# Kernel tuning notes

Measured on AMD Instinct MI355X. Metric: run time of the kernel, lower is better.

The kernel has to match this reference:

```python
import jax, jax.numpy as jnp
import numpy as np

NUM_HEADS = 8
NUM_LAYERS = 4
ATTN_DIM = 256
INPUT_DIM = 256
HEAD_DIM = ATTN_DIM // NUM_HEADS


def setup_inputs() -> dict:
    key = jax.random.key(0)
    ks = jax.random.split(key, 4)
    B, N = 32, 512
    agents_state = jax.random.normal(ks[0], (B, N, INPUT_DIM), dtype=jnp.float32)
    # normc_initializer(0.01): small std weights; bias zeros (torch default bias is
    # uniform but zeros suffice for a baseline; kept as explicit params)
    Wq = jax.random.normal(ks[1], (ATTN_DIM, INPUT_DIM), dtype=jnp.float32) * 0.01
    Wk = jax.random.normal(ks[2], (ATTN_DIM, INPUT_DIM), dtype=jnp.float32) * 0.01
    Wv = jax.random.normal(ks[3], (ATTN_DIM, INPUT_DIM), dtype=jnp.float32) * 0.01
    bq = jnp.zeros((ATTN_DIM,), dtype=jnp.float32)
    bk = jnp.zeros((ATTN_DIM,), dtype=jnp.float32)
    bv = jnp.zeros((ATTN_DIM,), dtype=jnp.float32)
    return {"agents_state": agents_state, "Wq": Wq, "bq": bq, "Wk": Wk, "bk": bk, "Wv": Wv, "bv": bv}


def _mha(q, k, v):
    # q: [B, N, D]; k, v: [B, M, D]
    B, N, _ = q.shape
    M = k.shape[1]
    qh = q.reshape(B, N, NUM_HEADS, HEAD_DIM)
    kh = k.reshape(B, M, NUM_HEADS, HEAD_DIM)
    vh = v.reshape(B, M, NUM_HEADS, HEAD_DIM)
    scores = jnp.einsum('bnhd,bmhd->bnhm', qh, kh) / np.float32(HEAD_DIM ** 0.5)
    attn = jax.nn.softmax(scores, axis=-1)
    out = jnp.einsum('bnhm,bmhd->bnhd', attn, vh)
    return out.reshape(B, N, ATTN_DIM)


def reference(agents_state, Wq, bq, Wk, bk, Wv, bv):
    queries = agents_state @ Wq.T + bq
    keys = agents_state @ Wk.T + bk
    values = agents_state @ Wv.T + bv
    attn_output = queries
    for _ in range(NUM_LAYERS):
        attn_output = attn_output + _mha(attn_output, keys, values)
    return attn_output
```

## Files before the change

kernel.cpp:

```cpp
#include <hip/hip_runtime.h>

typedef __bf16 bf16x8 __attribute__((ext_vector_type(8)));
typedef float  f32x4  __attribute__((ext_vector_type(4)));

#define K_SCALE 0.25505402682247326f

static __device__ __forceinline__ unsigned short f2bf(float f) {
  return __builtin_bit_cast(unsigned short, (__bf16)f);
}
static __device__ __forceinline__ f32x4 mfma16(bf16x8 a, bf16x8 b, f32x4 c) {
  return __builtin_amdgcn_mfma_f32_16x16x32_bf16(a, b, c, 0, 0, 0);
}

__global__ __launch_bounds__(256) void prep_kernel(
    const float* __restrict__ X,
    const float* __restrict__ Wq, const float* __restrict__ bq,
    const float* __restrict__ Wk, const float* __restrict__ bk,
    const float* __restrict__ Wv, const float* __restrict__ bv,
    unsigned short* __restrict__ Xb, unsigned short* __restrict__ Wf,
    float* __restrict__ bias) {
  int blk = blockIdx.x;
  if (blk < 1024) {
    int idx = blk * 4096 + threadIdx.x * 16;
    const float4* src = reinterpret_cast<const float4*>(X + idx);
    float4 f0 = src[0], f1 = src[1], f2 = src[2], f3 = src[3];
    bf16x8 h0, h1;
    h0[0]=(__bf16)f0.x; h0[1]=(__bf16)f0.y; h0[2]=(__bf16)f0.z; h0[3]=(__bf16)f0.w;
    h0[4]=(__bf16)f1.x; h0[5]=(__bf16)f1.y; h0[6]=(__bf16)f1.z; h0[7]=(__bf16)f1.w;
    h1[0]=(__bf16)f2.x; h1[1]=(__bf16)f2.y; h1[2]=(__bf16)f2.z; h1[3]=(__bf16)f2.w;
    h1[4]=(__bf16)f3.x; h1[5]=(__bf16)f3.y; h1[6]=(__bf16)f3.z; h1[7]=(__bf16)f3.w;
    *reinterpret_cast<bf16x8*>(Xb + idx) = h0;
    *reinterpret_cast<bf16x8*>(Xb + idx + 8) = h1;
    return;
  }
  if (blk == 1120) {
    int t = threadIdx.x;
#pragma unroll
    for (int kseg = 0; kseg < 3; ++kseg) {
      int i = kseg * 256 + t;
      float bb;
      if (i < 256)      bb = bq[i];
      else if (i < 512) bb = bk[i - 256] * K_SCALE;
      else              bb = bv[i - 512];
      bias[i] = bb;
    }
    return;
  }
  int fidx = (blk - 1024) * 256 + threadIdx.x;
  int lane = fidx & 63;
  int ks = (fidx >> 6) & 7;
  int ct = fidx >> 9;
  int n = ct * 16 + (lane & 15);
  int kk = ks * 32 + (lane >> 4) * 8;
  const float* src;
  float scale = 1.0f;
  if (n < 256)      src = Wq + n * 256 + kk;
  else if (n < 512) { src = Wk + (n - 256) * 256 + kk; scale = K_SCALE; }
  else              src = Wv + (n - 512) * 256 + kk;
  float4 f0 = reinterpret_cast<const float4*>(src)[0];
  float4 f1 = reinterpret_cast<const float4*>(src)[1];
  bf16x8 h;
  h[0] = (__bf16)(f0.x * scale); h[1] = (__bf16)(f0.y * scale);
  h[2] = (__bf16)(f0.z * scale); h[3] = (__bf16)(f0.w * scale);
  h[4] = (__bf16)(f1.x * scale); h[5] = (__bf16)(f1.y * scale);
  h[6] = (__bf16)(f1.z * scale); h[7] = (__bf16)(f1.w * scale);
  *reinterpret_cast<bf16x8*>(Wf + fidx * 8) = h;
}

__global__ __launch_bounds__(512, 4) void attn_kernel(
    const unsigned short* __restrict__ Xb, const unsigned short* __restrict__ Wf,
    const float* __restrict__ bias, float* __restrict__ Out) {
  __shared__ __align__(16) unsigned short Ks[16384];
  __shared__ __align__(16) unsigned short Vf[16384];
  const int tid = threadIdx.x;
  const int bh = blockIdx.x >> 1, seg = blockIdx.x & 1;
  const int b = bh >> 3, h = bh & 7;
  const int w = tid >> 6, lane = tid & 63, c = lane & 15, quad = lane >> 4;
  const f32x4 zf = {0.f, 0.f, 0.f, 0.f};
  const int kw = w * 64;
  f32x4 accK[2][4], accV[4][2];
#pragma unroll
  for (int dt = 0; dt < 2; ++dt)
#pragma unroll
    for (int kt = 0; kt < 4; ++kt) { accK[dt][kt] = zf; accV[kt][dt] = zf; }
#pragma unroll
  for (int ks = 0; ks < 8; ++ks) {
    bf16x8 bX[4];
#pragma unroll
    for (int kt = 0; kt < 4; ++kt)
      bX[kt] = *reinterpret_cast<const bf16x8*>(
          Xb + (b * 512 + kw + kt * 16 + c) * 256 + ks * 32 + quad * 8);
    bf16x8 aWk[2], aWv[2];
#pragma unroll
    for (int dt = 0; dt < 2; ++dt) {
      aWk[dt] = *reinterpret_cast<const bf16x8*>(
          Wf + (((16 + h * 2 + dt) * 8 + ks) * 64 + lane) * 8);
      aWv[dt] = *reinterpret_cast<const bf16x8*>(
          Wf + (((32 + h * 2 + dt) * 8 + ks) * 64 + lane) * 8);
    }
#pragma unroll
    for (int dt = 0; dt < 2; ++dt)
#pragma unroll
      for (int kt = 0; kt < 4; ++kt)
        accK[dt][kt] = mfma16(aWk[dt], bX[kt], accK[dt][kt]);
#pragma unroll
    for (int mt = 0; mt < 4; ++mt)
#pragma unroll
      for (int nt = 0; nt < 2; ++nt)
        accV[mt][nt] = mfma16(bX[mt], aWv[nt], accV[mt][nt]);
  }
#pragma unroll
  for (int dt = 0; dt < 2; ++dt) {
    f32x4 bk4 = *reinterpret_cast<const f32x4*>(bias + 256 + h * 32 + dt * 16 + quad * 4);
#pragma unroll
    for (int kt = 0; kt < 4; ++kt) {
      int n = kw + kt * 16 + c;
      int slot = quad ^ ((n >> 1) & 3);
      ushort4 pk;
      pk.x = f2bf(accK[dt][kt][0] + bk4[0]); pk.y = f2bf(accK[dt][kt][1] + bk4[1]);
      pk.z = f2bf(accK[dt][kt][2] + bk4[2]); pk.w = f2bf(accK[dt][kt][3] + bk4[3]);
      *reinterpret_cast<ushort4*>(&Ks[n * 32 + slot * 8 + dt * 4]) = pk;
    }
  }
#pragma unroll
  for (int nt = 0; nt < 2; ++nt) {
    float bv1 = bias[512 + h * 32 + nt * 16 + c];
#pragma unroll
    for (int mt = 0; mt < 4; ++mt) {
      ushort4 pk;
      pk.x = f2bf(accV[mt][nt][0] + bv1); pk.y = f2bf(accV[mt][nt][1] + bv1);
      pk.z = f2bf(accV[mt][nt][2] + bv1); pk.w = f2bf(accV[mt][nt][3] + bv1);
      *reinterpret_cast<ushort4*>(
          &Vf[((w * 2 + (mt >> 1)) * 2 + nt) * 512 + (quad * 16 + c) * 8 + (mt & 1) * 4]) = pk;
    }
  }
  const int rowq = seg * 256 + w * 32;
  f32x4 x[2][2] = {{zf, zf}, {zf, zf}};
#pragma unroll
  for (int ks = 0; ks < 8; ++ks) {
    bf16x8 bXq[2], aQ[2];
#pragma unroll
    for (int rg = 0; rg < 2; ++rg)
      bXq[rg] = *reinterpret_cast<const bf16x8*>(
          Xb + (b * 512 + rowq + rg * 16 + c) * 256 + ks * 32 + quad * 8);
#pragma unroll
    for (int tt = 0; tt < 2; ++tt)
      aQ[tt] = *reinterpret_cast<const bf16x8*>(
          Wf + (((h * 2 + tt) * 8 + ks) * 64 + lane) * 8);
#pragma unroll
    for (int rg = 0; rg < 2; ++rg)
#pragma unroll
      for (int tt = 0; tt < 2; ++tt)
        x[rg][tt] = mfma16(aQ[tt], bXq[rg], x[rg][tt]);
  }
#pragma unroll
  for (int tt = 0; tt < 2; ++tt) {
    f32x4 bq4 = *reinterpret_cast<const f32x4*>(bias + h * 32 + tt * 16 + quad * 4);
#pragma unroll
    for (int rg = 0; rg < 2; ++rg) x[rg][tt] += bq4;
  }
  __syncthreads();
  bf16x8 ones;
#pragma unroll
  for (int j = 0; j < 8; ++j) ones[j] = (__bf16)1.0f;
#pragma unroll 1
  for (int layer = 0; layer < 4; ++layer) {
    bf16x8 aq[2];
#pragma unroll
    for (int rg = 0; rg < 2; ++rg) {
      aq[rg][0] = (__bf16)x[rg][0][0]; aq[rg][1] = (__bf16)x[rg][0][1];
      aq[rg][2] = (__bf16)x[rg][0][2]; aq[rg][3] = (__bf16)x[rg][0][3];
      aq[rg][4] = (__bf16)x[rg][1][0]; aq[rg][5] = (__bf16)x[rg][1][1];
      aq[rg][6] = (__bf16)x[rg][1][2]; aq[rg][7] = (__bf16)x[rg][1][3];
    }
    f32x4 sacc[2] = {zf, zf};
    f32x4 O[2][2] = {{zf, zf}, {zf, zf}};
#pragma unroll 4
    for (int ch = 0; ch < 16; ++ch) {
      f32x4 S[2][2];
#pragma unroll
      for (int tt = 0; tt < 2; ++tt) {
        int n = (ch * 2 + tt) * 16 + c;
        bf16x8 kf = *reinterpret_cast<const bf16x8*>(
            &Ks[n * 32 + ((quad ^ ((n >> 1) & 3)) << 3)]);
#pragma unroll
        for (int rg = 0; rg < 2; ++rg) S[rg][tt] = mfma16(kf, aq[rg], zf);
      }
      bf16x8 ap[2];
#pragma unroll
      for (int rg = 0; rg < 2; ++rg) {
#pragma unroll
        for (int tt = 0; tt < 2; ++tt)
#pragma unroll
          for (int r = 0; r < 4; ++r)
            S[rg][tt][r] = __builtin_amdgcn_exp2f(S[rg][tt][r]);
        ap[rg][0] = (__bf16)S[rg][0][0]; ap[rg][1] = (__bf16)S[rg][0][1];
        ap[rg][2] = (__bf16)S[rg][0][2]; ap[rg][3] = (__bf16)S[rg][0][3];
        ap[rg][4] = (__bf16)S[rg][1][0]; ap[rg][5] = (__bf16)S[rg][1][1];
        ap[rg][6] = (__bf16)S[rg][1][2]; ap[rg][7] = (__bf16)S[rg][1][3];
        sacc[rg] = mfma16(ones, ap[rg], sacc[rg]);
      }
#pragma unroll
      for (int tt = 0; tt < 2; ++tt) {
        bf16x8 vf = *reinterpret_cast<const bf16x8*>(
            &Vf[((ch * 2 + tt) * 64 + lane) * 8]);
#pragma unroll
        for (int rg = 0; rg < 2; ++rg) O[rg][tt] = mfma16(vf, ap[rg], O[rg][tt]);
      }
    }
#pragma unroll
    for (int rg = 0; rg < 2; ++rg) {
      float inv = __builtin_amdgcn_rcpf(sacc[rg][0]);
#pragma unroll
      for (int tt = 0; tt < 2; ++tt)
#pragma unroll
        for (int r = 0; r < 4; ++r) x[rg][tt][r] += O[rg][tt][r] * inv;
    }
  }
#pragma unroll
  for (int rg = 0; rg < 2; ++rg)
#pragma unroll
    for (int tt = 0; tt < 2; ++tt)
      *reinterpret_cast<f32x4*>(
          Out + (b * 512 + rowq + rg * 16 + c) * 256 + h * 32 + tt * 16 + quad * 4) = x[rg][tt];
}

extern "C" void kernel_launch(void* const* d_in, const int* in_sizes, int n_in,
                              void* d_out, int out_size, void* d_ws, size_t ws_size,
                              hipStream_t stream) {
  const float* X  = (const float*)d_in[0];
  const float* Wq = (const float*)d_in[1];
  const float* bq = (const float*)d_in[2];
  const float* Wk = (const float*)d_in[3];
  const float* bk = (const float*)d_in[4];
  const float* Wv = (const float*)d_in[5];
  const float* bv = (const float*)d_in[6];
  char* ws = (char*)d_ws;
  unsigned short* Wf   = (unsigned short*)(ws);
  float*          bias = (float*)(ws + 393216);
  unsigned short* Xb   = (unsigned short*)(ws + 397312);
  float* out = (float*)d_out;
  prep_kernel<<<1121, 256, 0, stream>>>(X, Wq, bq, Wk, bk, Wv, bv, Xb, Wf, bias);
  attn_kernel<<<512, 512, 0, stream>>>(Xb, Wf, bias, out);
}
```

Baseline: 153.2 us.

## Split K/V projection into separate phases and remap block order by batch

The fused K and V projection loop becomes two sequential scoped phases separated by scheduling barriers, so each phase holds only one set of accumulators and register pressure drops under the 4-blocks-per-CU bound. This reloads the X tiles from global memory twice, once per phase. The block index mapping also changes so that consecutive blocks take different batches for the same head and segment, which alters L2 reuse of the weight tiles versus the X tiles.

```diff
diff --git a/kernel.cpp b/kernel.cpp
--- a/kernel.cpp
+++ b/kernel.cpp
@@ -73,67 +73,88 @@
   __shared__ __align__(16) unsigned short Ks[16384];
   __shared__ __align__(16) unsigned short Vf[16384];
   const int tid = threadIdx.x;
-  const int bh = blockIdx.x >> 1, seg = blockIdx.x & 1;
-  const int b = bh >> 3, h = bh & 7;
+  const int b = blockIdx.x & 31, hs = blockIdx.x >> 5;
+  const int h = hs >> 1, seg = hs & 1;
   const int w = tid >> 6, lane = tid & 63, c = lane & 15, quad = lane >> 4;
   const f32x4 zf = {0.f, 0.f, 0.f, 0.f};
   const int kw = w * 64;
-  f32x4 accK[2][4], accV[4][2];
-#pragma unroll
-  for (int dt = 0; dt < 2; ++dt)
-#pragma unroll
-    for (int kt = 0; kt < 4; ++kt) { accK[dt][kt] = zf; accV[kt][dt] = zf; }
-#pragma unroll
-  for (int ks = 0; ks < 8; ++ks) {
-    bf16x8 bX[4];
-#pragma unroll
-    for (int kt = 0; kt < 4; ++kt)
-      bX[kt] = *reinterpret_cast<const bf16x8*>(
-          Xb + (b * 512 + kw + kt * 16 + c) * 256 + ks * 32 + quad * 8);
-    bf16x8 aWk[2], aWv[2];
+  {
+    f32x4 accK[2][4];
+#pragma unroll
+    for (int dt = 0; dt < 2; ++dt)
+#pragma unroll
+      for (int kt = 0; kt < 4; ++kt) accK[dt][kt] = zf;
+#pragma unroll
+    for (int ks = 0; ks < 8; ++ks) {
+      bf16x8 bX[4];
+#pragma unroll
+      for (int kt = 0; kt < 4; ++kt)
+        bX[kt] = *reinterpret_cast<const bf16x8*>(
+            Xb + (b * 512 + kw + kt * 16 + c) * 256 + ks * 32 + quad * 8);
+      bf16x8 aWk[2];
+#pragma unroll
+      for (int dt = 0; dt < 2; ++dt)
+        aWk[dt] = *reinterpret_cast<const bf16x8*>(
+            Wf + (((16 + h * 2 + dt) * 8 + ks) * 64 + lane) * 8);
+#pragma unroll
+      for (int dt = 0; dt < 2; ++dt)
+#pragma unroll
+        for (int kt = 0; kt < 4; ++kt)
+          accK[dt][kt] = mfma16(aWk[dt], bX[kt], accK[dt][kt]);
+    }
 #pragma unroll
     for (int dt = 0; dt < 2; ++dt) {
-      aWk[dt] = *reinterpret_cast<const bf16x8*>(
-          Wf + (((16 + h * 2 + dt) * 8 + ks) * 64 + lane) * 8);
-      aWv[dt] = *reinterpret_cast<const bf16x8*>(
-          Wf + (((32 + h * 2 + dt) * 8 + ks) * 64 + lane) * 8);
-    }
-#pragma unroll
-    for (int dt = 0; dt < 2; ++dt)
-#pragma unroll
-      for (int kt = 0; kt < 4; ++kt)
-        accK[dt][kt] = mfma16(aWk[dt], bX[kt], accK[dt][kt]);
+      f32x4 bk4 = *reinterpret_cast<const f32x4*>(bias + 256 + h * 32 + dt * 16 + quad * 4);
+#pragma unroll
+      for (int kt = 0; kt < 4; ++kt) {
+        int n = kw + kt * 16 + c;
+        int slot = quad ^ ((n >> 1) & 3);
+        ushort4 pk;
+        pk.x = f2bf(accK[dt][kt][0] + bk4[0]); pk.y = f2bf(accK[dt][kt][1] + bk4[1]);
+        pk.z = f2bf(accK[dt][kt][2] + bk4[2]); pk.w = f2bf(accK[dt][kt][3] + bk4[3]);
+        *reinterpret_cast<ushort4*>(&Ks[n * 32 + slot * 8 + dt * 4]) = pk;
+      }
+    }
+  }
+  __builtin_amdgcn_sched_barrier(0);
+  {
+    f32x4 accV[4][2];
 #pragma unroll
     for (int mt = 0; mt < 4; ++mt)
 #pragma unroll
+      for (int nt = 0; nt < 2; ++nt) accV[mt][nt] = zf;
+#pragma unroll
+    for (int ks = 0; ks < 8; ++ks) {
+      bf16x8 bX[4];
+#pragma unroll
+      for (int mt = 0; mt < 4; ++mt)
+        bX[mt] = *reinterpret_cast<const bf16x8*>(
+            Xb + (b * 512 + kw + mt * 16 + c) * 256 + ks * 32 + quad * 8);
+      bf16x8 aWv[2];
+#pragma unroll
       for (int nt = 0; nt < 2; ++nt)
-        accV[mt][nt] = mfma16(bX[mt], aWv[nt], accV[mt][nt]);
-  }
-#pragma unroll
-  for (int dt = 0; dt < 2; ++dt) {
-    f32x4 bk4 = *reinterpret_cast<const f32x4*>(bias + 256 + h * 32 + dt * 16 + quad * 4);
-#pragma unroll
-    for (int kt = 0; kt < 4; ++kt) {
-      int n = kw + kt * 16 + c;
-      int slot = quad ^ ((n >> 1) & 3);
-      ushort4 pk;
-      pk.x = f2bf(accK[dt][kt][0] + bk4[0]); pk.y = f2bf(accK[dt][kt][1] + bk4[1]);
-      pk.z = f2bf(accK[dt][kt][2] + bk4[2]); pk.w = f2bf(accK[dt][kt][3] + bk4[3]);
-      *reinterpret_cast<ushort4*>(&Ks[n * 32 + slot * 8 + dt * 4]) = pk;
-    }
-  }
-#pragma unroll
-  for (int nt = 0; nt < 2; ++nt) {
-    float bv1 = bias[512 + h * 32 + nt * 16 + c];
-#pragma unroll
-    for (int mt = 0; mt < 4; ++mt) {
-      ushort4 pk;
-      pk.x = f2bf(accV[mt][nt][0] + bv1); pk.y = f2bf(accV[mt][nt][1] + bv1);
-      pk.z = f2bf(accV[mt][nt][2] + bv1); pk.w = f2bf(accV[mt][nt][3] + bv1);
-      *reinterpret_cast<ushort4*>(
-          &Vf[((w * 2 + (mt >> 1)) * 2 + nt) * 512 + (quad * 16 + c) * 8 + (mt & 1) * 4]) = pk;
-    }
-  }
+        aWv[nt] = *reinterpret_cast<const bf16x8*>(
+            Wf + (((32 + h * 2 + nt) * 8 + ks) * 64 + lane) * 8);
+#pragma unroll
+      for (int mt = 0; mt < 4; ++mt)
+#pragma unroll
+        for (int nt = 0; nt < 2; ++nt)
+          accV[mt][nt] = mfma16(bX[mt], aWv[nt], accV[mt][nt]);
+    }
+#pragma unroll
+    for (int nt = 0; nt < 2; ++nt) {
+      float bv1 = bias[512 + h * 32 + nt * 16 + c];
+#pragma unroll
+      for (int mt = 0; mt < 4; ++mt) {
+        ushort4 pk;
+        pk.x = f2bf(accV[mt][nt][0] + bv1); pk.y = f2bf(accV[mt][nt][1] + bv1);
+        pk.z = f2bf(accV[mt][nt][2] + bv1); pk.w = f2bf(accV[mt][nt][3] + bv1);
+        *reinterpret_cast<ushort4*>(
+            &Vf[((w * 2 + (mt >> 1)) * 2 + nt) * 512 + (quad * 16 + c) * 8 + (mt & 1) * 4]) = pk;
+      }
+    }
+  }
+  __builtin_amdgcn_sched_barrier(0);
   const int rowq = seg * 256 + w * 32;
   f32x4 x[2][2] = {{zf, zf}, {zf, zf}};
 #pragma unroll
```

Measured after the change: 155.4 us. Within noise of the previous version (+1.4%).
